# Kernel tuning notes

Hardware: AMD Instinct MI355X
Metric: run time of the kernel (lower is better)

Reference implementation:

```python
import jax, jax.numpy as jnp
import numpy as np

B, S, DIN, DEG = 256, 51, 512, 50
N = B * S           # 13056 nodes
E = N * DEG         # 652800 edges
NEG_SLOPE = 0.01    # torch leaky_relu default
EPS = 1e-12         # torch F.normalize default eps


def setup_inputs() -> dict:
    key = jax.random.key(0)
    ks = iter(jax.random.split(key, 64))

    def p(shape):
        fan_in = shape[0] if len(shape) > 1 else shape[0]
        return jax.random.normal(next(ks), shape, jnp.float32) / np.sqrt(fan_in)

    inp = {
        "x": jax.random.normal(next(ks), (B, S, DIN), jnp.float32),
        "x_pose": jax.random.normal(next(ks), (B, S, 7), jnp.float32),
        # mlp2: in_feats->256->128->64 (ReLU)
        "m2w1": p((DIN, 256)), "m2b1": jnp.zeros((256,), jnp.float32),
        "m2w2": p((256, 128)), "m2b2": jnp.zeros((128,), jnp.float32),
        "m2w3": p((128, 64)),  "m2b3": jnp.zeros((64,), jnp.float32),
        # mlp3: 7->16->32->64 (ReLU)
        "m3w1": p((7, 16)),   "m3b1": jnp.zeros((16,), jnp.float32),
        "m3w2": p((16, 32)),  "m3b2": jnp.zeros((32,), jnp.float32),
        "m3w3": p((32, 64)),  "m3b3": jnp.zeros((64,), jnp.float32),
        # Encoder: 128->256 (ReLU)
        "encw": p((128, 256)), "encb": jnp.zeros((256,), jnp.float32),
        # edge MLP: 256->256->128->64->1 (leaky_relu, sigmoid at end)
        "ew1": p((256, 256)), "eb1": jnp.zeros((256,), jnp.float32),
        "ew2": p((256, 128)), "eb2": jnp.zeros((128,), jnp.float32),
        "ew3": p((128, 64)),  "eb3": jnp.zeros((64,), jnp.float32),
        "ew4": p((64, 1)),    "eb4": jnp.zeros((1,), jnp.float32),
        # SAGEConv(256,128,'mean'): fc_self, fc_neigh, bias
        "wself": p((256, 128)), "wneigh": p((256, 128)),
        "sageb": jnp.zeros((128,), jnp.float32),
        # Decoder: 128->7
        "decw": p((128, 7)), "decb": jnp.zeros((7,), jnp.float32),
        # graph edges (src -> dst)
        "edge_src": jax.random.randint(next(ks), (E,), 0, N, jnp.int32),
        "edge_dst": jax.random.randint(next(ks), (E,), 0, N, jnp.int32),
    }
    return inp


def reference(x, x_pose,
              m2w1, m2b1, m2w2, m2b2, m2w3, m2b3,
              m3w1, m3b1, m3w2, m3b2, m3w3, m3b3,
              encw, encb,
              ew1, eb1, ew2, eb2, ew3, eb3, ew4, eb4,
              wself, wneigh, sageb, decw, decb,
              edge_src, edge_dst):
    relu = jax.nn.relu
    lrelu = lambda h: jax.nn.leaky_relu(h, NEG_SLOPE)

    # node feature encoders
    h = relu(relu(relu(x @ m2w1 + m2b1) @ m2w2 + m2b2) @ m2w3 + m2b3)        # [B,S,64]
    hp = relu(relu(relu(x_pose @ m3w1 + m3b1) @ m3w2 + m3b2) @ m3w3 + m3b3)  # [B,S,64]
    xn = relu(jnp.concatenate([h, hp], axis=2) @ encw + encb)                # [B,S,256]
    xn = xn.reshape(N, 256)                                                  # node feats

    # apply_edges: score = sigmoid(MLP(h_u - h_v))
    d = xn[edge_src] - xn[edge_dst]                                          # [E,256]
    s = lrelu(d @ ew1 + eb1)
    s = lrelu(s @ ew2 + eb2)
    s = lrelu(s @ ew3 + eb3)
    e = jax.nn.sigmoid(s @ ew4 + eb4)                                        # [E,1]

    # SAGEConv mean aggregation with edge weights: mean over in-edges of e*h_u
    msg = e * xn[edge_src]                                                   # [E,256]
    neigh_sum = jax.ops.segment_sum(msg, edge_dst, num_segments=N)           # [N,256]
    deg = jax.ops.segment_sum(jnp.ones((E,), jnp.float32), edge_dst, num_segments=N)
    neigh = neigh_sum / jnp.maximum(deg, 1.0)[:, None]                       # zero-deg -> 0
    A = xn @ wself + neigh @ wneigh + sageb                                  # [N,128]
    A = A.reshape(B, S, 128)

    est_pose = A @ decw + decb                                               # [B,S,7]
    pos_out = est_pose[:, 0, :3]
    ori_out = est_pose[:, 0, 3:]

    A = lrelu(A)
    A = A / jnp.maximum(jnp.linalg.norm(A, axis=1, keepdims=True), EPS)      # F.normalize dim=1
    return (A, e, pos_out, ori_out)
```

## Files before the change

### kernel.cpp

```cpp
#include <hip/hip_runtime.h>
#include <math.h>

#define B_ 256
#define S_ 51
#define NN (B_*S_)
#define DEG_ 50
#define EE (NN*DEG_)
#define NEG_SLOPE 0.01f
#define EPS_ 1e-12f

#define A_SIZE (NN*128)
#define E_OFF  A_SIZE
#define POS_OFF (A_SIZE + EE)
#define ORI_OFF (POS_OFF + B_*3)

typedef __bf16 bf16x8 __attribute__((ext_vector_type(8)));
typedef __bf16 bf16x4 __attribute__((ext_vector_type(4)));
typedef float  f32x4  __attribute__((ext_vector_type(4)));

typedef __attribute__((address_space(1))) const void GVoid;
typedef __attribute__((address_space(3))) void LVoid;

__device__ __forceinline__ float act_apply(float v, int ACT) {
    if (ACT == 1) return fmaxf(v, 0.0f);
    if (ACT == 2) return v > 0.0f ? v : NEG_SLOPE * v;
    return v;
}

template<int ACT, int ACC>
__global__ __launch_bounds__(256) void gemm_kernel(
    const float* __restrict__ A, int lda,
    const float* __restrict__ W, int ldw,
    const float* __restrict__ bias,
    float* __restrict__ C, int ldc,
    int M, int K, int N)
{
    __shared__ float As[32][68];
    __shared__ float Ws[32][68];

    const int tid = threadIdx.x;
    const int tx = tid & 15;
    const int ty = tid >> 4;
    const int m0 = blockIdx.x * 64;
    const int n0 = blockIdx.y * 64;

    float acc[4][4];
#pragma unroll
    for (int i = 0; i < 4; ++i)
#pragma unroll
        for (int j = 0; j < 4; ++j) acc[i][j] = 0.0f;

    const int ktiles = (K + 31) >> 5;
    for (int kt = 0; kt < ktiles; ++kt) {
        const int k0 = kt << 5;
#pragma unroll
        for (int it = 0; it < 8; ++it) {
            int idx = tid + it * 256;
            int kk = idx & 31;
            int r  = idx >> 5;
            float v = 0.0f;
            int gr = m0 + r, gk = k0 + kk;
            if (gr < M && gk < K) v = A[(size_t)gr * lda + gk];
            As[kk][r] = v;
        }
#pragma unroll
        for (int it = 0; it < 8; ++it) {
            int idx = tid + it * 256;
            int c  = idx & 63;
            int kk = idx >> 6;
            float v = 0.0f;
            int gk = k0 + kk, gc = n0 + c;
            if (gk < K && gc < N) v = W[(size_t)gk * ldw + gc];
            Ws[kk][c] = v;
        }
        __syncthreads();
#pragma unroll
        for (int kk = 0; kk < 32; ++kk) {
            float4 av = *(const float4*)&As[kk][ty * 4];
            float4 wv = *(const float4*)&Ws[kk][tx * 4];
            float a[4] = {av.x, av.y, av.z, av.w};
            float w[4] = {wv.x, wv.y, wv.z, wv.w};
#pragma unroll
            for (int i = 0; i < 4; ++i)
#pragma unroll
                for (int j = 0; j < 4; ++j)
                    acc[i][j] = fmaf(a[i], w[j], acc[i][j]);
        }
        __syncthreads();
    }

#pragma unroll
    for (int i = 0; i < 4; ++i) {
        int row = m0 + ty * 4 + i;
        if (row >= M) continue;
#pragma unroll
        for (int j = 0; j < 4; ++j) {
            int col = n0 + tx * 4 + j;
            if (col >= N) continue;
            float v = acc[i][j];
            if (bias) v += bias[col];
            if (ACC) v += C[(size_t)row * ldc + col];
            C[(size_t)row * ldc + col] = act_apply(v, ACT);
        }
    }
}

__global__ __launch_bounds__(256) void pack_w_kernel(
    const float* __restrict__ W, __bf16* __restrict__ Wp, int K, int N)
{
    int t = blockIdx.x * 256 + threadIdx.x;
    if (t >= K * N) return;
    int j    = t & 7;
    int lane = (t >> 3) & 63;
    int rkt  = t >> 9;
    int KT = K >> 5;
    int kt = rkt % KT;
    int cf = rkt / KT;
    int k = kt * 32 + (lane >> 4) * 8 + j;
    int n = cf * 16 + (lane & 15);
    Wp[t] = (__bf16)W[(size_t)k * N + n];
}

__global__ __launch_bounds__(256) void pack_w2_kernel(
    const float* __restrict__ W, __bf16* __restrict__ Wph, __bf16* __restrict__ Wpl,
    int K, int N)
{
    int t = blockIdx.x * 256 + threadIdx.x;
    if (t >= K * N) return;
    int j    = t & 7;
    int lane = (t >> 3) & 63;
    int rkt  = t >> 9;
    int KT = K >> 5;
    int kt = rkt % KT;
    int cf = rkt / KT;
    int k = kt * 32 + (lane >> 4) * 8 + j;
    int n = cf * 16 + (lane & 15);
    float v = W[(size_t)k * N + n];
    __bf16 h = (__bf16)v;
    Wph[t] = h;
    Wpl[t] = (__bf16)(v - (float)h);
}

template<int K, int BN>
__global__ __launch_bounds__(256) void ygemm_kernel(
    const __bf16* __restrict__ A, const __bf16* __restrict__ Wp,
    __bf16* __restrict__ C, int ldc)
{
    constexpr int NCF = BN / 16;
    __shared__ __bf16 As[128 * 32];

    const int tid  = threadIdx.x;
    const int lane = tid & 63;
    const int w    = tid >> 6;
    const int lg   = lane >> 4;
    const int li   = lane & 15;
    const int n_blk = blockIdx.x * BN;
    const int m_blk = blockIdx.y * 128;

    f32x4 acc[2][NCF];
#pragma unroll
    for (int mf = 0; mf < 2; ++mf)
#pragma unroll
        for (int cf = 0; cf < NCF; ++cf)
#pragma unroll
            for (int r = 0; r < 4; ++r) acc[mf][cf][r] = 0.0f;

    const __bf16* WpBase = Wp + ((size_t)(n_blk / 16) * (K / 32)) * 512 + (size_t)lane * 8;

    for (int kt = 0; kt < K / 32; ++kt) {
#pragma unroll
        for (int i = 0; i < 2; ++i) {
            int slot0 = i * 256 + w * 64;
            int s  = slot0 + lane;
            int r  = s >> 2;
            int sl = s & 3;
            int kb = sl ^ ((r >> 1) & 3);
            const __bf16* g = A + (size_t)(m_blk + r) * K + kt * 32 + kb * 8;
            __builtin_amdgcn_global_load_lds((GVoid*)g,
                                             (LVoid*)((char*)As + (size_t)slot0 * 16),
                                             16, 0, 0);
        }
        bf16x8 bf[NCF];
        const __bf16* Wb = WpBase + (size_t)kt * 512;
#pragma unroll
        for (int cf = 0; cf < NCF; ++cf)
            bf[cf] = *(const bf16x8*)(Wb + (size_t)cf * (K / 32) * 512);

        __syncthreads();

        bf16x8 af[2];
#pragma unroll
        for (int mf = 0; mf < 2; ++mf) {
            int row = w * 32 + mf * 16 + li;
            int sl  = lg ^ ((row >> 1) & 3);
            af[mf] = *(const bf16x8*)((const char*)As + (size_t)row * 64 + sl * 16);
        }
#pragma unroll
        for (int mf = 0; mf < 2; ++mf)
#pragma unroll
            for (int cf = 0; cf < NCF; ++cf)
                acc[mf][cf] = __builtin_amdgcn_mfma_f32_16x16x32_bf16(
                    af[mf], bf[cf], acc[mf][cf], 0, 0, 0);
        __syncthreads();
    }

#pragma unroll
    for (int mf = 0; mf < 2; ++mf) {
        int row0 = m_blk + w * 32 + mf * 16 + lg * 4;
#pragma unroll
        for (int cf = 0; cf < NCF; ++cf) {
            int col = n_blk + cf * 16 + li;
#pragma unroll
            for (int r = 0; r < 4; ++r)
                C[(size_t)(row0 + r) * ldc + col] = (__bf16)acc[mf][cf][r];
        }
    }
}

__global__ __launch_bounds__(256) void edge_full_kernel(
    const __bf16* __restrict__ Yb, const float* __restrict__ eb1,
    const int* __restrict__ src, const int* __restrict__ dst,
    const __bf16* __restrict__ Wp2, const float* __restrict__ eb2,
    const __bf16* __restrict__ Wp3, const float* __restrict__ eb3,
    const float* __restrict__ ew4, const float* __restrict__ eb4,
    float* __restrict__ e_out)
{
    constexpr int K = 256, NCF = 8;
    __shared__ __bf16 As[128 * 32];
    __shared__ __bf16 S2[128 * 128];

    const int tid  = threadIdx.x;
    const int lane = tid & 63;
    const int w    = tid >> 6;
    const int lg   = lane >> 4;
    const int li   = lane & 15;
    const int m_blk = blockIdx.x * 128;

    const int sr = tid >> 1;
    const int sh = tid & 1;
    const int e  = m_blk + sr;
    const __bf16* ys = Yb + (size_t)src[e] * 256;
    const __bf16* yd = Yb + (size_t)dst[e] * 256;
    const int swz = (sr >> 1) & 3;
    char* wp0 = (char*)As + sr * 64 + (((sh * 2)     ^ swz) * 16);
    char* wp1 = (char*)As + sr * 64 + (((sh * 2 + 1) ^ swz) * 16);

    f32x4 acc[2][NCF];
#pragma unroll
    for (int mf = 0; mf < 2; ++mf)
#pragma unroll
        for (int cf = 0; cf < NCF; ++cf)
#pragma unroll
            for (int r = 0; r < 4; ++r) acc[mf][cf][r] = 0.0f;

    const __bf16* WpBase2 = Wp2 + (size_t)lane * 8;

    for (int kt = 0; kt < K / 32; ++kt) {
        const int k0 = kt * 32 + sh * 16;
        bf16x8 a0 = *(const bf16x8*)(ys + k0);
        bf16x8 a1 = *(const bf16x8*)(ys + k0 + 8);
        bf16x8 b0 = *(const bf16x8*)(yd + k0);
        bf16x8 b1 = *(const bf16x8*)(yd + k0 + 8);
        bf16x8 o0, o1;
#pragma unroll
        for (int j = 0; j < 8; ++j) {
            float v0 = (float)a0[j] - (float)b0[j] + eb1[k0 + j];
            float v1 = (float)a1[j] - (float)b1[j] + eb1[k0 + 8 + j];
            v0 = v0 > 0.0f ? v0 : NEG_SLOPE * v0;
            v1 = v1 > 0.0f ? v1 : NEG_SLOPE * v1;
            o0[j] = (__bf16)v0;
            o1[j] = (__bf16)v1;
        }
        *(bf16x8*)wp0 = o0;
        *(bf16x8*)wp1 = o1;

        bf16x8 bf[NCF];
        const __bf16* Wb = WpBase2 + (size_t)kt * 512;
#pragma unroll
        for (int cf = 0; cf < NCF; ++cf)
            bf[cf] = *(const bf16x8*)(Wb + (size_t)cf * (K / 32) * 512);

        __syncthreads();

        bf16x8 af[2];
#pragma unroll
        for (int mf = 0; mf < 2; ++mf) {
            int row = w * 32 + mf * 16 + li;
            int sl  = lg ^ ((row >> 1) & 3);
            af[mf] = *(const bf16x8*)((const char*)As + (size_t)row * 64 + sl * 16);
        }
#pragma unroll
        for (int mf = 0; mf < 2; ++mf)
#pragma unroll
            for (int cf = 0; cf < NCF; ++cf)
                acc[mf][cf] = __builtin_amdgcn_mfma_f32_16x16x32_bf16(
                    af[mf], bf[cf], acc[mf][cf], 0, 0, 0);
        __syncthreads();
    }

#pragma unroll
    for (int mf = 0; mf < 2; ++mf) {
        int row0 = w * 32 + mf * 16 + lg * 4;
#pragma unroll
        for (int cf = 0; cf < NCF; ++cf) {
            int col = cf * 16 + li;
            float bv = eb2[col];
            int sl = col >> 3;
            int sb = col & 7;
#pragma unroll
            for (int r = 0; r < 4; ++r) {
                int row = row0 + r;
                float v = acc[mf][cf][r] + bv;
                v = v > 0.0f ? v : NEG_SLOPE * v;
                S2[row * 128 + ((sl ^ (row & 7)) << 3) + sb] = (__bf16)v;
            }
        }
    }
    __syncthreads();

    constexpr int NCF3 = 4;
    f32x4 acc3[2][NCF3];
#pragma unroll
    for (int mf = 0; mf < 2; ++mf)
#pragma unroll
        for (int cf = 0; cf < NCF3; ++cf)
#pragma unroll
            for (int r = 0; r < 4; ++r) acc3[mf][cf][r] = 0.0f;

    const __bf16* WpBase3 = Wp3 + (size_t)lane * 8;
#pragma unroll
    for (int kt = 0; kt < 4; ++kt) {
        bf16x8 af[2];
#pragma unroll
        for (int mf = 0; mf < 2; ++mf) {
            int row = w * 32 + mf * 16 + li;
            int sl  = (kt * 4 + lg) ^ (row & 7);
            af[mf] = *(const bf16x8*)&S2[row * 128 + (sl << 3)];
        }
        bf16x8 bf[NCF3];
        const __bf16* Wb = WpBase3 + (size_t)kt * 512;
#pragma unroll
        for (int cf = 0; cf < NCF3; ++cf)
            bf[cf] = *(const bf16x8*)(Wb + (size_t)cf * 4 * 512);
#pragma unroll
        for (int mf = 0; mf < 2; ++mf)
#pragma unroll
            for (int cf = 0; cf < NCF3; ++cf)
                acc3[mf][cf] = __builtin_amdgcn_mfma_f32_16x16x32_bf16(
                    af[mf], bf[cf], acc3[mf][cf], 0, 0, 0);
    }

    float p[2][4];
#pragma unroll
    for (int mf = 0; mf < 2; ++mf)
#pragma unroll
        for (int r = 0; r < 4; ++r) p[mf][r] = 0.0f;
#pragma unroll
    for (int cf = 0; cf < NCF3; ++cf) {
        int col = cf * 16 + li;
        float b3 = eb3[col];
        float w4 = ew4[col];
#pragma unroll
        for (int mf = 0; mf < 2; ++mf)
#pragma unroll
            for (int r = 0; r < 4; ++r) {
                float v = acc3[mf][cf][r] + b3;
                v = v > 0.0f ? v : NEG_SLOPE * v;
                p[mf][r] = fmaf(v, w4, p[mf][r]);
            }
    }
#pragma unroll
    for (int mf = 0; mf < 2; ++mf)
#pragma unroll
        for (int r = 0; r < 4; ++r) {
#pragma unroll
            for (int m = 1; m < 16; m <<= 1)
                p[mf][r] += __shfl_xor(p[mf][r], m, 16);
        }
    if (li == 0) {
        float b4 = eb4[0];
#pragma unroll
        for (int mf = 0; mf < 2; ++mf)
#pragma unroll
            for (int r = 0; r < 4; ++r) {
                int ei = m_blk + w * 32 + mf * 16 + lg * 4 + r;
                float ev = 1.0f / (1.0f + expf(-(p[mf][r] + b4)));
                e_out[ei] = ev;
            }
    }
}

template<int K, int BN, int ACT, int OUT, int ACC>
__global__ __launch_bounds__(256) void mmx_kernel(
    const __bf16* __restrict__ Ah, const __bf16* __restrict__ Al,
    const __bf16* __restrict__ Wph, const __bf16* __restrict__ Wpl,
    const float* __restrict__ bias,
    float* __restrict__ Cf, __bf16* __restrict__ Ch, __bf16* __restrict__ Cl, int ldc)
{
    constexpr int NCF = BN / 16;
    __shared__ __bf16 AsH[128 * 32];
    __shared__ __bf16 AsL[128 * 32];

    const int tid  = threadIdx.x;
    const int lane = tid & 63;
    const int w    = tid >> 6;
    const int lg   = lane >> 4;
    const int li   = lane & 15;
    const int n_blk = blockIdx.x * BN;
    const int m_blk = blockIdx.y * 128;

    f32x4 acc[2][NCF];
#pragma unroll
    for (int mf = 0; mf < 2; ++mf)
#pragma unroll
        for (int cf = 0; cf < NCF; ++cf)
#pragma unroll
            for (int r = 0; r < 4; ++r) acc[mf][cf][r] = 0.0f;

    const size_t wbase = ((size_t)(n_blk / 16) * (K / 32)) * 512 + (size_t)lane * 8;

    for (int kt = 0; kt < K / 32; ++kt) {
#pragma unroll
        for (int i = 0; i < 2; ++i) {
            int slot0 = i * 256 + w * 64;
            int s  = slot0 + lane;
            int r  = s >> 2;
            int sl = s & 3;
            int kb = sl ^ ((r >> 1) & 3);
            size_t goff = (size_t)(m_blk + r) * K + kt * 32 + kb * 8;
            __builtin_amdgcn_global_load_lds((GVoid*)(Ah + goff),
                                             (LVoid*)((char*)AsH + (size_t)slot0 * 16),
                                             16, 0, 0);
            __builtin_amdgcn_global_load_lds((GVoid*)(Al + goff),
                                             (LVoid*)((char*)AsL + (size_t)slot0 * 16),
                                             16, 0, 0);
        }
        bf16x8 bfh[NCF], bfl[NCF];
        const size_t wo = wbase + (size_t)kt * 512;
#pragma unroll
        for (int cf = 0; cf < NCF; ++cf) {
            size_t o = wo + (size_t)cf * (K / 32) * 512;
            bfh[cf] = *(const bf16x8*)(Wph + o);
            bfl[cf] = *(const bf16x8*)(Wpl + o);
        }

        __syncthreads();

        bf16x8 afh[2], afl[2];
#pragma unroll
        for (int mf = 0; mf < 2; ++mf) {
            int row = w * 32 + mf * 16 + li;
            int sl  = lg ^ ((row >> 1) & 3);
            afh[mf] = *(const bf16x8*)((const char*)AsH + (size_t)row * 64 + sl * 16);
            afl[mf] = *(const bf16x8*)((const char*)AsL + (size_t)row * 64 + sl * 16);
        }
#pragma unroll
        for (int mf = 0; mf < 2; ++mf)
#pragma unroll
            for (int cf = 0; cf < NCF; ++cf) {
                acc[mf][cf] = __builtin_amdgcn_mfma_f32_16x16x32_bf16(
                    afh[mf], bfh[cf], acc[mf][cf], 0, 0, 0);
                acc[mf][cf] = __builtin_amdgcn_mfma_f32_16x16x32_bf16(
                    afh[mf], bfl[cf], acc[mf][cf], 0, 0, 0);
                acc[mf][cf] = __builtin_amdgcn_mfma_f32_16x16x32_bf16(
                    afl[mf], bfh[cf], acc[mf][cf], 0, 0, 0);
            }
        __syncthreads();
    }

    float bv[NCF];
#pragma unroll
    for (int cf = 0; cf < NCF; ++cf) bv[cf] = bias ? bias[n_blk + cf * 16 + li] : 0.0f;
#pragma unroll
    for (int mf = 0; mf < 2; ++mf) {
        int row0 = m_blk + w * 32 + mf * 16 + lg * 4;
#pragma unroll
        for (int cf = 0; cf < NCF; ++cf) {
            int col = n_blk + cf * 16 + li;
#pragma unroll
            for (int r = 0; r < 4; ++r) {
                float v = acc[mf][cf][r] + bv[cf];
                size_t idx = (size_t)(row0 + r) * ldc + col;
                if (ACC) v += Cf[idx];
                v = act_apply(v, ACT);
                if (OUT & 1) Cf[idx] = v;
                if (OUT & 2) {
                    __bf16 h = (__bf16)v;
                    Ch[idx] = h;
                    Cl[idx] = (__bf16)(v - (float)h);
                }
            }
        }
    }
}

__global__ __launch_bounds__(256) void split_bf16_kernel(
    const float* __restrict__ in, __bf16* __restrict__ hi, __bf16* __restrict__ lo, int n8)
{
    int i = blockIdx.x * 256 + threadIdx.x;
    if (i >= n8) return;
    const float4* p = (const float4*)in + (size_t)i * 2;
    float4 a = p[0], b = p[1];
    float v[8] = {a.x, a.y, a.z, a.w, b.x, b.y, b.z, b.w};
    bf16x8 oh, ol;
#pragma unroll
    for (int j = 0; j < 8; ++j) {
        __bf16 h = (__bf16)v[j];
        oh[j] = h;
        ol[j] = (__bf16)(v[j] - (float)h);
    }
    *(bf16x8*)(hi + (size_t)i * 8) = oh;
    *(bf16x8*)(lo + (size_t)i * 8) = ol;
}

__global__ __launch_bounds__(256) void hist_kernel(
    const int* __restrict__ dst, int* __restrict__ counts)
{
    int e = blockIdx.x * 256 + threadIdx.x;
    if (e < EE) atomicAdd(&counts[dst[e]], 1);
}

__global__ __launch_bounds__(1024) void scan_kernel(
    const int* __restrict__ counts, int* __restrict__ row_start, int* __restrict__ cursor)
{
    __shared__ int buf[1024];
    __shared__ int carry_s;
    int tid = threadIdx.x;
    if (tid == 0) carry_s = 0;
    __syncthreads();
    for (int t0 = 0; t0 < NN; t0 += 1024) {
        int i = t0 + tid;
        int v = (i < NN) ? counts[i] : 0;
        buf[tid] = v;
        __syncthreads();
        int c = carry_s;
        for (int o = 1; o < 1024; o <<= 1) {
            int u = (tid >= o) ? buf[tid - o] : 0;
            __syncthreads();
            buf[tid] += u;
            __syncthreads();
        }
        int excl = buf[tid] - v;
        if (i < NN) { row_start[i] = c + excl; cursor[i] = c + excl; }
        int total = buf[1023];
        __syncthreads();
        if (tid == 0) carry_s = c + total;
        __syncthreads();
    }
}

__global__ __launch_bounds__(256) void scatter_kernel(
    const int* __restrict__ src, const int* __restrict__ dst,
    const float* __restrict__ e_out, int* __restrict__ cursor, int2* __restrict__ bucket)
{
    int e = blockIdx.x * 256 + threadIdx.x;
    if (e >= EE) return;
    int d = dst[e];
    int pos = atomicAdd(&cursor[d], 1);
    bucket[pos] = make_int2(src[e], __float_as_int(e_out[e]));
}

__global__ __launch_bounds__(256) void neigh_gather_kernel(
    const float* __restrict__ xn, const int2* __restrict__ bucket,
    const int* __restrict__ row_start, const int* __restrict__ counts,
    __bf16* __restrict__ nh, __bf16* __restrict__ nl)
{
    __shared__ int2 eb[128];
    int n = blockIdx.x;
    int f = threadIdx.x;
    int s0 = row_start[n];
    int cnt = counts[n];
    float acc = 0.0f;
    for (int t = 0; t < cnt; t += 128) {
        int m = (cnt - t < 128) ? (cnt - t) : 128;
        __syncthreads();
        if (f < m) eb[f] = bucket[s0 + t + f];
        __syncthreads();
        for (int i = 0; i < m; ++i) {
            int2 p = eb[i];
            acc = fmaf(__int_as_float(p.y), xn[(size_t)p.x * 256 + f], acc);
        }
    }
    float dv = (float)(cnt > 0 ? cnt : 1);
    float v = acc / dv;
    __bf16 h = (__bf16)v;
    nh[(size_t)n * 256 + f] = h;
    nl[(size_t)n * 256 + f] = (__bf16)(v - (float)h);
}

__global__ __launch_bounds__(128) void pose_kernel(
    const float* __restrict__ A_pre, const float* __restrict__ decw,
    const float* __restrict__ decb, float* __restrict__ pos, float* __restrict__ ori)
{
    __shared__ float arow[128];
    int b = blockIdx.x;
    arow[threadIdx.x] = A_pre[(size_t)(b * S_) * 128 + threadIdx.x];
    __syncthreads();
    int t = threadIdx.x;
    if (t < 7) {
        float s = decb[t];
        for (int c = 0; c < 128; ++c) s = fmaf(arow[c], decw[c * 7 + t], s);
        if (t < 3) pos[b * 3 + t] = s;
        else       ori[b * 4 + (t - 3)] = s;
    }
}

__global__ __launch_bounds__(128) void norm_kernel(
    const float* __restrict__ A_pre, float* __restrict__ out)
{
    int b = blockIdx.x;
    int c = threadIdx.x;
    size_t base = (size_t)b * S_ * 128 + c;
    float ss = 0.0f;
    for (int s = 0; s < S_; ++s) {
        float v = A_pre[base + (size_t)s * 128];
        v = v > 0.0f ? v : NEG_SLOPE * v;
        ss = fmaf(v, v, ss);
    }
    float nrm = fmaxf(sqrtf(ss), EPS_);
    float inv = 1.0f / nrm;
    for (int s = 0; s < S_; ++s) {
        float v = A_pre[base + (size_t)s * 128];
        v = v > 0.0f ? v : NEG_SLOPE * v;
        out[base + (size_t)s * 128] = v * inv;
    }
}

extern "C" void kernel_launch(void* const* d_in, const int* in_sizes, int n_in,
                              void* d_out, int out_size, void* d_ws, size_t ws_size,
                              hipStream_t stream) {
    const float* x      = (const float*)d_in[0];
    const float* x_pose = (const float*)d_in[1];
    const float* m2w1 = (const float*)d_in[2];
    const float* m2b1 = (const float*)d_in[3];
    const float* m2w2 = (const float*)d_in[4];
    const float* m2b2 = (const float*)d_in[5];
    const float* m2w3 = (const float*)d_in[6];
    const float* m2b3 = (const float*)d_in[7];
    const float* m3w1 = (const float*)d_in[8];
    const float* m3b1 = (const float*)d_in[9];
    const float* m3w2 = (const float*)d_in[10];
    const float* m3b2 = (const float*)d_in[11];
    const float* m3w3 = (const float*)d_in[12];
    const float* m3b3 = (const float*)d_in[13];
    const float* encw = (const float*)d_in[14];
    const float* encb = (const float*)d_in[15];
    const float* ew1  = (const float*)d_in[16];
    const float* eb1  = (const float*)d_in[17];
    const float* ew2  = (const float*)d_in[18];
    const float* eb2  = (const float*)d_in[19];
    const float* ew3  = (const float*)d_in[20];
    const float* eb3  = (const float*)d_in[21];
    const float* ew4  = (const float*)d_in[22];
    const float* eb4  = (const float*)d_in[23];
    const float* wself  = (const float*)d_in[24];
    const float* wneigh = (const float*)d_in[25];
    const float* sageb  = (const float*)d_in[26];
    const float* decw = (const float*)d_in[27];
    const float* decb = (const float*)d_in[28];
    const int* esrc = (const int*)d_in[29];
    const int* edst = (const int*)d_in[30];
    float* out = (float*)d_out;

    char* base = (char*)d_ws;
    size_t off = 0;
    auto alloc = [&](size_t bytes) { char* p = base + off; off += (bytes + 15) & ~15ULL; return p; };
    float* xn        = (float*)alloc((size_t)NN * 256 * 4);
    float* A_pre     = (float*)alloc((size_t)NN * 128 * 4);
    float* p1        = (float*)alloc((size_t)NN * 16 * 4);
    float* p2        = (float*)alloc((size_t)NN * 32 * 4);
    int*  counts    = (int*)alloc((size_t)NN * 4);
    int*  row_start = (int*)alloc((size_t)NN * 4);
    int*  cursor    = (int*)alloc((size_t)NN * 4);
    int2* bucket    = (int2*)alloc((size_t)EE * 8);
    __bf16* Yb   = (__bf16*)alloc((size_t)NN * 256 * 2);
    __bf16* xh   = (__bf16*)alloc((size_t)NN * 512 * 2);
    __bf16* xl   = (__bf16*)alloc((size_t)NN * 512 * 2);
    __bf16* t1h  = (__bf16*)alloc((size_t)NN * 256 * 2);
    __bf16* t1l  = (__bf16*)alloc((size_t)NN * 256 * 2);
    __bf16* t2h  = (__bf16*)alloc((size_t)NN * 128 * 2);
    __bf16* t2l  = (__bf16*)alloc((size_t)NN * 128 * 2);
    __bf16* hch  = (__bf16*)alloc((size_t)NN * 128 * 2);
    __bf16* hcl  = (__bf16*)alloc((size_t)NN * 128 * 2);
    __bf16* p2h  = (__bf16*)alloc((size_t)NN * 32 * 2);
    __bf16* p2l  = (__bf16*)alloc((size_t)NN * 32 * 2);
    __bf16* xnh  = (__bf16*)alloc((size_t)NN * 256 * 2);
    __bf16* xnl  = (__bf16*)alloc((size_t)NN * 256 * 2);
    __bf16* ngh  = (__bf16*)alloc((size_t)NN * 256 * 2);
    __bf16* ngl  = (__bf16*)alloc((size_t)NN * 256 * 2);
    __bf16* wpn1h = (__bf16*)alloc((size_t)512 * 256 * 2);
    __bf16* wpn1l = (__bf16*)alloc((size_t)512 * 256 * 2);
    __bf16* wpn2h = (__bf16*)alloc((size_t)256 * 128 * 2);
    __bf16* wpn2l = (__bf16*)alloc((size_t)256 * 128 * 2);
    __bf16* wpn3h = (__bf16*)alloc((size_t)128 * 64 * 2);
    __bf16* wpn3l = (__bf16*)alloc((size_t)128 * 64 * 2);
    __bf16* wpp3h = (__bf16*)alloc((size_t)32 * 64 * 2);
    __bf16* wpp3l = (__bf16*)alloc((size_t)32 * 64 * 2);
    __bf16* wpenh = (__bf16*)alloc((size_t)128 * 256 * 2);
    __bf16* wpenl = (__bf16*)alloc((size_t)128 * 256 * 2);
    __bf16* wpsfh = (__bf16*)alloc((size_t)256 * 128 * 2);
    __bf16* wpsfl = (__bf16*)alloc((size_t)256 * 128 * 2);
    __bf16* wpngh = (__bf16*)alloc((size_t)256 * 128 * 2);
    __bf16* wpngl = (__bf16*)alloc((size_t)256 * 128 * 2);
    __bf16* wpe1 = (__bf16*)alloc((size_t)256 * 256 * 2);
    __bf16* wpe2 = (__bf16*)alloc((size_t)256 * 128 * 2);
    __bf16* wpe3 = (__bf16*)alloc((size_t)128 * 64 * 2);

    hipMemsetAsync(counts, 0, (size_t)NN * sizeof(int), stream);

    pack_w2_kernel<<<(512*256+255)/256, 256, 0, stream>>>(m2w1, wpn1h, wpn1l, 512, 256);
    pack_w2_kernel<<<(256*128+255)/256, 256, 0, stream>>>(m2w2, wpn2h, wpn2l, 256, 128);
    pack_w2_kernel<<<(128*64 +255)/256, 256, 0, stream>>>(m2w3, wpn3h, wpn3l, 128, 64);
    pack_w2_kernel<<<(32*64  +255)/256, 256, 0, stream>>>(m3w3, wpp3h, wpp3l, 32, 64);
    pack_w2_kernel<<<(128*256+255)/256, 256, 0, stream>>>(encw, wpenh, wpenl, 128, 256);
    pack_w2_kernel<<<(256*128+255)/256, 256, 0, stream>>>(wself, wpsfh, wpsfl, 256, 128);
    pack_w2_kernel<<<(256*128+255)/256, 256, 0, stream>>>(wneigh, wpngh, wpngl, 256, 128);
    pack_w_kernel<<<(256*256+255)/256, 256, 0, stream>>>(ew1, wpe1, 256, 256);
    pack_w_kernel<<<(256*128+255)/256, 256, 0, stream>>>(ew2, wpe2, 256, 128);
    pack_w_kernel<<<(128*64 +255)/256, 256, 0, stream>>>(ew3, wpe3, 128, 64);

    split_bf16_kernel<<<(NN*512/8 + 255)/256, 256, 0, stream>>>(x, xh, xl, NN*512/8);

    const dim3 blk(256, 1, 1);
    const int MB = NN / 128;

    mmx_kernel<512,64,1,2,0><<<dim3(4, MB), blk, 0, stream>>>(xh, xl, wpn1h, wpn1l, m2b1, nullptr, t1h, t1l, 256);
    mmx_kernel<256,64,1,2,0><<<dim3(2, MB), blk, 0, stream>>>(t1h, t1l, wpn2h, wpn2l, m2b2, nullptr, t2h, t2l, 128);
    mmx_kernel<128,64,1,2,0><<<dim3(1, MB), blk, 0, stream>>>(t2h, t2l, wpn3h, wpn3l, m2b3, nullptr, hch, hcl, 128);

    gemm_kernel<1,0><<<dim3((NN+63)/64, 1), blk, 0, stream>>>(x_pose, 7,  m3w1, 16, m3b1, p1, 16, NN, 7, 16);
    gemm_kernel<1,0><<<dim3((NN+63)/64, 1), blk, 0, stream>>>(p1,    16,  m3w2, 32, m3b2, p2, 32, NN, 16, 32);
    split_bf16_kernel<<<(NN*32/8 + 255)/256, 256, 0, stream>>>(p2, p2h, p2l, NN*32/8);
    mmx_kernel< 32,64,1,2,0><<<dim3(1, MB), blk, 0, stream>>>(p2h, p2l, wpp3h, wpp3l, m3b3, nullptr, hch + 64, hcl + 64, 128);

    mmx_kernel<128,64,1,3,0><<<dim3(4, MB), blk, 0, stream>>>(hch, hcl, wpenh, wpenl, encb, xn, xnh, xnl, 256);

    ygemm_kernel<256,128><<<dim3(2, MB), blk, 0, stream>>>(xnh, wpe1, Yb, 256);

    edge_full_kernel<<<dim3(EE / 128), blk, 0, stream>>>(
        Yb, eb1, esrc, edst, wpe2, eb2, wpe3, eb3, ew4, eb4, out + E_OFF);

    hist_kernel<<<(EE + 255) / 256, 256, 0, stream>>>(edst, counts);
    scan_kernel<<<1, 1024, 0, stream>>>(counts, row_start, cursor);
    scatter_kernel<<<(EE + 255) / 256, 256, 0, stream>>>(esrc, edst, out + E_OFF, cursor, bucket);
    neigh_gather_kernel<<<NN, 256, 0, stream>>>(xn, bucket, row_start, counts, ngh, ngl);

    mmx_kernel<256,64,0,1,0><<<dim3(2, MB), blk, 0, stream>>>(xnh, xnl, wpsfh, wpsfl, sageb,  A_pre, nullptr, nullptr, 128);
    mmx_kernel<256,64,0,1,1><<<dim3(2, MB), blk, 0, stream>>>(ngh, ngl, wpngh, wpngl, nullptr, A_pre, nullptr, nullptr, 128);

    pose_kernel<<<B_, 128, 0, stream>>>(A_pre, decw, decb, out + POS_OFF, out + ORI_OFF);
    norm_kernel<<<B_, 128, 0, stream>>>(A_pre, out);
}
```

Measured before the change: 632.0 us.

## Batch weight packing, fuse pose MLP, load edge MFMA operands directly

The ten weight-packing launches become one kernel driven by a descriptor table. The two small pose-MLP GEMMs and the split kernel become one per-node kernel that writes the bf16 hi/lo parts directly. In the edge kernel, each lane now builds its MFMA A fragments straight from the gathered Y rows, so the shared-memory staging tile and two barriers per k-step go away. The goal is fewer launches and less LDS traffic and synchronisation, at the cost of more redundant global gather loads per lane.

```diff
diff --git a/kernel.cpp b/kernel.cpp
--- a/kernel.cpp
+++ b/kernel.cpp
@@ -27,118 +27,59 @@
     return v;
 }
 
-template<int ACT, int ACC>
-__global__ __launch_bounds__(256) void gemm_kernel(
-    const float* __restrict__ A, int lda,
-    const float* __restrict__ W, int ldw,
-    const float* __restrict__ bias,
-    float* __restrict__ C, int ldc,
-    int M, int K, int N)
-{
-    __shared__ float As[32][68];
-    __shared__ float Ws[32][68];
-
-    const int tid = threadIdx.x;
-    const int tx = tid & 15;
-    const int ty = tid >> 4;
-    const int m0 = blockIdx.x * 64;
-    const int n0 = blockIdx.y * 64;
-
-    float acc[4][4];
-#pragma unroll
-    for (int i = 0; i < 4; ++i)
-#pragma unroll
-        for (int j = 0; j < 4; ++j) acc[i][j] = 0.0f;
-
-    const int ktiles = (K + 31) >> 5;
-    for (int kt = 0; kt < ktiles; ++kt) {
-        const int k0 = kt << 5;
-#pragma unroll
-        for (int it = 0; it < 8; ++it) {
-            int idx = tid + it * 256;
-            int kk = idx & 31;
-            int r  = idx >> 5;
-            float v = 0.0f;
-            int gr = m0 + r, gk = k0 + kk;
-            if (gr < M && gk < K) v = A[(size_t)gr * lda + gk];
-            As[kk][r] = v;
-        }
-#pragma unroll
-        for (int it = 0; it < 8; ++it) {
-            int idx = tid + it * 256;
-            int c  = idx & 63;
-            int kk = idx >> 6;
-            float v = 0.0f;
-            int gk = k0 + kk, gc = n0 + c;
-            if (gk < K && gc < N) v = W[(size_t)gk * ldw + gc];
-            Ws[kk][c] = v;
-        }
-        __syncthreads();
-#pragma unroll
-        for (int kk = 0; kk < 32; ++kk) {
-            float4 av = *(const float4*)&As[kk][ty * 4];
-            float4 wv = *(const float4*)&Ws[kk][tx * 4];
-            float a[4] = {av.x, av.y, av.z, av.w};
-            float w[4] = {wv.x, wv.y, wv.z, wv.w};
-#pragma unroll
-            for (int i = 0; i < 4; ++i)
-#pragma unroll
-                for (int j = 0; j < 4; ++j)
-                    acc[i][j] = fmaf(a[i], w[j], acc[i][j]);
-        }
-        __syncthreads();
-    }
-
-#pragma unroll
-    for (int i = 0; i < 4; ++i) {
-        int row = m0 + ty * 4 + i;
-        if (row >= M) continue;
-#pragma unroll
-        for (int j = 0; j < 4; ++j) {
-            int col = n0 + tx * 4 + j;
-            if (col >= N) continue;
-            float v = acc[i][j];
-            if (bias) v += bias[col];
-            if (ACC) v += C[(size_t)row * ldc + col];
-            C[(size_t)row * ldc + col] = act_apply(v, ACT);
-        }
-    }
-}
-
-__global__ __launch_bounds__(256) void pack_w_kernel(
-    const float* __restrict__ W, __bf16* __restrict__ Wp, int K, int N)
-{
-    int t = blockIdx.x * 256 + threadIdx.x;
-    if (t >= K * N) return;
+struct PackDesc { const float* src; __bf16* dh; __bf16* dl; int kts; int N; int start; };
+struct PackArgs { PackDesc d[10]; int total; };
+
+__global__ __launch_bounds__(256) void pack_all_kernel(PackArgs a)
+{
+    int idx = blockIdx.x * 256 + threadIdx.x;
+    if (idx >= a.total) return;
+    int e = 0;
+    while (e < 9 && idx >= a.d[e + 1].start) ++e;
+    PackDesc pd = a.d[e];
+    int t = idx - pd.start;
     int j    = t & 7;
     int lane = (t >> 3) & 63;
     int rkt  = t >> 9;
-    int KT = K >> 5;
-    int kt = rkt % KT;
-    int cf = rkt / KT;
+    int kt = rkt & ((1 << pd.kts) - 1);
+    int cf = rkt >> pd.kts;
     int k = kt * 32 + (lane >> 4) * 8 + j;
     int n = cf * 16 + (lane & 15);
-    Wp[t] = (__bf16)W[(size_t)k * N + n];
-}
-
-__global__ __launch_bounds__(256) void pack_w2_kernel(
-    const float* __restrict__ W, __bf16* __restrict__ Wph, __bf16* __restrict__ Wpl,
-    int K, int N)
-{
-    int t = blockIdx.x * 256 + threadIdx.x;
-    if (t >= K * N) return;
-    int j    = t & 7;
-    int lane = (t >> 3) & 63;
-    int rkt  = t >> 9;
-    int KT = K >> 5;
-    int kt = rkt % KT;
-    int cf = rkt / KT;
-    int k = kt * 32 + (lane >> 4) * 8 + j;
-    int n = cf * 16 + (lane & 15);
-    float v = W[(size_t)k * N + n];
+    float v = pd.src[(size_t)k * pd.N + n];
     __bf16 h = (__bf16)v;
-    Wph[t] = h;
-    Wpl[t] = (__bf16)(v - (float)h);
+    pd.dh[t] = h;
+    if (pd.dl) pd.dl[t] = (__bf16)(v - (float)h);
+}
+
+__global__ __launch_bounds__(256) void pose_fused_kernel(
+    const float* __restrict__ xp,
+    const float* __restrict__ w1, const float* __restrict__ b1,
+    const float* __restrict__ w2, const float* __restrict__ b2,
+    __bf16* __restrict__ p2h, __bf16* __restrict__ p2l)
+{
+    int n = blockIdx.x * 256 + threadIdx.x;
+    if (n >= NN) return;
+    float xv[7];
+#pragma unroll
+    for (int c = 0; c < 7; ++c) xv[c] = xp[(size_t)n * 7 + c];
+    float p1[16];
+#pragma unroll
+    for (int j = 0; j < 16; ++j) {
+        float s = b1[j];
+#pragma unroll
+        for (int c = 0; c < 7; ++c) s = fmaf(xv[c], w1[c * 16 + j], s);
+        p1[j] = fmaxf(s, 0.0f);
+    }
+#pragma unroll
+    for (int j = 0; j < 32; ++j) {
+        float s = b2[j];
+#pragma unroll
+        for (int c = 0; c < 16; ++c) s = fmaf(p1[c], w2[c * 32 + j], s);
+        s = fmaxf(s, 0.0f);
+        __bf16 h = (__bf16)s;
+        p2h[(size_t)n * 32 + j] = h;
+        p2l[(size_t)n * 32 + j] = (__bf16)(s - (float)h);
+    }
 }
 
 template<int K, int BN>
@@ -225,8 +166,7 @@
     const float* __restrict__ ew4, const float* __restrict__ eb4,
     float* __restrict__ e_out)
 {
-    constexpr int K = 256, NCF = 8;
-    __shared__ __bf16 As[128 * 32];
+    constexpr int NCF = 8;
     __shared__ __bf16 S2[128 * 128];
 
     const int tid  = threadIdx.x;
@@ -236,14 +176,13 @@
     const int li   = lane & 15;
     const int m_blk = blockIdx.x * 128;
 
-    const int sr = tid >> 1;
-    const int sh = tid & 1;
-    const int e  = m_blk + sr;
-    const __bf16* ys = Yb + (size_t)src[e] * 256;
-    const __bf16* yd = Yb + (size_t)dst[e] * 256;
-    const int swz = (sr >> 1) & 3;
-    char* wp0 = (char*)As + sr * 64 + (((sh * 2)     ^ swz) * 16);
-    char* wp1 = (char*)As + sr * 64 + (((sh * 2 + 1) ^ swz) * 16);
+    const int row0 = w * 32 + li;
+    const int row1 = row0 + 16;
+    const __bf16* ys0 = Yb + (size_t)src[m_blk + row0] * 256;
+    const __bf16* yd0 = Yb + (size_t)dst[m_blk + row0] * 256;
+    const __bf16* ys1 = Yb + (size_t)src[m_blk + row1] * 256;
+    const __bf16* yd1 = Yb + (size_t)dst[m_blk + row1] * 256;
+    const int ko = lg * 8;
 
     f32x4 acc[2][NCF];
 #pragma unroll
@@ -255,52 +194,36 @@
 
     const __bf16* WpBase2 = Wp2 + (size_t)lane * 8;
 
-    for (int kt = 0; kt < K / 32; ++kt) {
-        const int k0 = kt * 32 + sh * 16;
-        bf16x8 a0 = *(const bf16x8*)(ys + k0);
-        bf16x8 a1 = *(const bf16x8*)(ys + k0 + 8);
-        bf16x8 b0 = *(const bf16x8*)(yd + k0);
-        bf16x8 b1 = *(const bf16x8*)(yd + k0 + 8);
-        bf16x8 o0, o1;
+#pragma unroll
+    for (int kt = 0; kt < 8; ++kt) {
+        const int k0 = kt * 32 + ko;
+        bf16x8 a0 = *(const bf16x8*)(ys0 + k0);
+        bf16x8 b0 = *(const bf16x8*)(yd0 + k0);
+        bf16x8 a1 = *(const bf16x8*)(ys1 + k0);
+        bf16x8 b1 = *(const bf16x8*)(yd1 + k0);
+        bf16x8 af0, af1;
 #pragma unroll
         for (int j = 0; j < 8; ++j) {
-            float v0 = (float)a0[j] - (float)b0[j] + eb1[k0 + j];
-            float v1 = (float)a1[j] - (float)b1[j] + eb1[k0 + 8 + j];
+            float bias = eb1[k0 + j];
+            float v0 = (float)a0[j] - (float)b0[j] + bias;
+            float v1 = (float)a1[j] - (float)b1[j] + bias;
             v0 = v0 > 0.0f ? v0 : NEG_SLOPE * v0;
             v1 = v1 > 0.0f ? v1 : NEG_SLOPE * v1;
-            o0[j] = (__bf16)v0;
-            o1[j] = (__bf16)v1;
-        }
-        *(bf16x8*)wp0 = o0;
-        *(bf16x8*)wp1 = o1;
-
-        bf16x8 bf[NCF];
+            af0[j] = (__bf16)v0;
+            af1[j] = (__bf16)v1;
+        }
         const __bf16* Wb = WpBase2 + (size_t)kt * 512;
 #pragma unroll
-        for (int cf = 0; cf < NCF; ++cf)
-            bf[cf] = *(const bf16x8*)(Wb + (size_t)cf * (K / 32) * 512);
-
-        __syncthreads();
-
-        bf16x8 af[2];
-#pragma unroll
-        for (int mf = 0; mf < 2; ++mf) {
-            int row = w * 32 + mf * 16 + li;
-            int sl  = lg ^ ((row >> 1) & 3);
-            af[mf] = *(const bf16x8*)((const char*)As + (size_t)row * 64 + sl * 16);
-        }
-#pragma unroll
-        for (int mf = 0; mf < 2; ++mf)
-#pragma unroll
-            for (int cf = 0; cf < NCF; ++cf)
-                acc[mf][cf] = __builtin_amdgcn_mfma_f32_16x16x32_bf16(
-                    af[mf], bf[cf], acc[mf][cf], 0, 0, 0);
-        __syncthreads();
+        for (int cf = 0; cf < NCF; ++cf) {
+            bf16x8 bf = *(const bf16x8*)(Wb + (size_t)cf * 8 * 512);
+            acc[0][cf] = __builtin_amdgcn_mfma_f32_16x16x32_bf16(af0, bf, acc[0][cf], 0, 0, 0);
+            acc[1][cf] = __builtin_amdgcn_mfma_f32_16x16x32_bf16(af1, bf, acc[1][cf], 0, 0, 0);
+        }
     }
 
 #pragma unroll
     for (int mf = 0; mf < 2; ++mf) {
-        int row0 = w * 32 + mf * 16 + lg * 4;
+        int r0 = w * 32 + mf * 16 + lg * 4;
 #pragma unroll
         for (int cf = 0; cf < NCF; ++cf) {
             int col = cf * 16 + li;
@@ -309,7 +232,7 @@
             int sb = col & 7;
 #pragma unroll
             for (int r = 0; r < 4; ++r) {
-                int row = row0 + r;
+                int row = r0 + r;
                 float v = acc[mf][cf][r] + bv;
                 v = v > 0.0f ? v : NEG_SLOPE * v;
                 S2[row * 128 + ((sl ^ (row & 7)) << 3) + sb] = (__bf16)v;
@@ -667,8 +590,6 @@
     auto alloc = [&](size_t bytes) { char* p = base + off; off += (bytes + 15) & ~15ULL; return p; };
     float* xn        = (float*)alloc((size_t)NN * 256 * 4);
     float* A_pre     = (float*)alloc((size_t)NN * 128 * 4);
-    float* p1        = (float*)alloc((size_t)NN * 16 * 4);
-    float* p2        = (float*)alloc((size_t)NN * 32 * 4);
     int*  counts    = (int*)alloc((size_t)NN * 4);
     int*  row_start = (int*)alloc((size_t)NN * 4);
     int*  cursor    = (int*)alloc((size_t)NN * 4);
@@ -708,18 +629,29 @@
 
     hipMemsetAsync(counts, 0, (size_t)NN * sizeof(int), stream);
 
-    pack_w2_kernel<<<(512*256+255)/256, 256, 0, stream>>>(m2w1, wpn1h, wpn1l, 512, 256);
-    pack_w2_kernel<<<(256*128+255)/256, 256, 0, stream>>>(m2w2, wpn2h, wpn2l, 256, 128);
-    pack_w2_kernel<<<(128*64 +255)/256, 256, 0, stream>>>(m2w3, wpn3h, wpn3l, 128, 64);
-    pack_w2_kernel<<<(32*64  +255)/256, 256, 0, stream>>>(m3w3, wpp3h, wpp3l, 32, 64);
-    pack_w2_kernel<<<(128*256+255)/256, 256, 0, stream>>>(encw, wpenh, wpenl, 128, 256);
-    pack_w2_kernel<<<(256*128+255)/256, 256, 0, stream>>>(wself, wpsfh, wpsfl, 256, 128);
-    pack_w2_kernel<<<(256*128+255)/256, 256, 0, stream>>>(wneigh, wpngh, wpngl, 256, 128);
-    pack_w_kernel<<<(256*256+255)/256, 256, 0, stream>>>(ew1, wpe1, 256, 256);
-    pack_w_kernel<<<(256*128+255)/256, 256, 0, stream>>>(ew2, wpe2, 256, 128);
-    pack_w_kernel<<<(128*64 +255)/256, 256, 0, stream>>>(ew3, wpe3, 128, 64);
+    PackArgs pa;
+    int st = 0;
+    auto addp = [&](int i, const float* s, __bf16* dh, __bf16* dl, int K, int N) {
+        int kts = 0;
+        while ((32 << kts) < K) ++kts;
+        pa.d[i] = PackDesc{s, dh, dl, kts, N, st};
+        st += K * N;
+    };
+    addp(0, m2w1,  wpn1h, wpn1l, 512, 256);
+    addp(1, m2w2,  wpn2h, wpn2l, 256, 128);
+    addp(2, m2w3,  wpn3h, wpn3l, 128, 64);
+    addp(3, m3w3,  wpp3h, wpp3l, 32, 64);
+    addp(4, encw,  wpenh, wpenl, 128, 256);
+    addp(5, wself, wpsfh, wpsfl, 256, 128);
+    addp(6, wneigh,wpngh, wpngl, 256, 128);
+    addp(7, ew1,   wpe1,  nullptr, 256, 256);
+    addp(8, ew2,   wpe2,  nullptr, 256, 128);
+    addp(9, ew3,   wpe3,  nullptr, 128, 64);
+    pa.total = st;
+    pack_all_kernel<<<(st + 255) / 256, 256, 0, stream>>>(pa);
 
     split_bf16_kernel<<<(NN*512/8 + 255)/256, 256, 0, stream>>>(x, xh, xl, NN*512/8);
+    pose_fused_kernel<<<NN / 256, 256, 0, stream>>>(x_pose, m3w1, m3b1, m3w2, m3b2, p2h, p2l);
 
     const dim3 blk(256, 1, 1);
     const int MB = NN / 128;
@@ -727,10 +659,6 @@
     mmx_kernel<512,64,1,2,0><<<dim3(4, MB), blk, 0, stream>>>(xh, xl, wpn1h, wpn1l, m2b1, nullptr, t1h, t1l, 256);
     mmx_kernel<256,64,1,2,0><<<dim3(2, MB), blk, 0, stream>>>(t1h, t1l, wpn2h, wpn2l, m2b2, nullptr, t2h, t2l, 128);
     mmx_kernel<128,64,1,2,0><<<dim3(1, MB), blk, 0, stream>>>(t2h, t2l, wpn3h, wpn3l, m2b3, nullptr, hch, hcl, 128);
-
-    gemm_kernel<1,0><<<dim3((NN+63)/64, 1), blk, 0, stream>>>(x_pose, 7,  m3w1, 16, m3b1, p1, 16, NN, 7, 16);
-    gemm_kernel<1,0><<<dim3((NN+63)/64, 1), blk, 0, stream>>>(p1,    16,  m3w2, 32, m3b2, p2, 32, NN, 16, 32);
-    split_bf16_kernel<<<(NN*32/8 + 255)/256, 256, 0, stream>>>(p2, p2h, p2l, NN*32/8);
     mmx_kernel< 32,64,1,2,0><<<dim3(1, MB), blk, 0, stream>>>(p2h, p2l, wpp3h, wpp3l, m3b3, nullptr, hch + 64, hcl + 64, 128);
 
     mmx_kernel<128,64,1,3,0><<<dim3(4, MB), blk, 0, stream>>>(hch, hcl, wpenh, wpenl, encb, xn, xnh, xnl, 256);
```

Result: faster. 580.9 us (-8.1%).
